# Kernel tuning notes

Measured on AMD Instinct MI355X. Metric: run time of the kernel, lower is better.

The kernel has to match this reference:

```python
import jax, jax.numpy as jnp
import numpy as np

N_USERS, N_ITEMS = 100000, 100000
N_NODES = N_USERS + N_ITEMS
N_EDGES = 4000000
USER_DIM, ITEM_DIM = 256, 128
COMMON, HIDDEN, OUT = 64, 64, 32


def setup_inputs() -> dict:
    key = jax.random.key(0)
    ks = jax.random.split(key, 12)
    inp = {
        "user_tensor": jax.random.normal(ks[0], (N_USERS, USER_DIM), jnp.float32),
        "item_tensor": jax.random.normal(ks[1], (N_ITEMS, ITEM_DIM), jnp.float32),
        "edge_index": jax.random.randint(ks[2], (2, N_EDGES), 0, N_NODES, jnp.int64),
        "edge_weight": jax.random.uniform(ks[3], (N_EDGES,), jnp.float32),
        # user_proj / item_proj (nn.Linear: y = x @ W + b)
        "Wu": jax.random.normal(ks[4], (USER_DIM, COMMON), jnp.float32) / np.sqrt(USER_DIM),
        "bu": jnp.zeros((COMMON,), jnp.float32),
        "Wi": jax.random.normal(ks[5], (ITEM_DIM, COMMON), jnp.float32) / np.sqrt(ITEM_DIM),
        "bi": jnp.zeros((COMMON,), jnp.float32),
        # GCNConv layers (linear without bias + separate bias)
        "W1": jax.random.normal(ks[6], (COMMON, HIDDEN), jnp.float32) / np.sqrt(COMMON),
        "b1": jnp.zeros((HIDDEN,), jnp.float32),
        "W2": jax.random.normal(ks[7], (HIDDEN, OUT), jnp.float32) / np.sqrt(HIDDEN),
        "b2": jnp.zeros((OUT,), jnp.float32),
    }
    return inp


def gcn_conv(x, W, b, src, dst, ew, num_nodes):
    """PyG GCNConv: add self-loops (weight 1), symmetric deg norm, transform, scatter-add."""
    x = x @ W  # transform first: [N, out]
    loop = jnp.arange(num_nodes, dtype=src.dtype)
    src2 = jnp.concatenate([src, loop])
    dst2 = jnp.concatenate([dst, loop])
    ew2 = jnp.concatenate([ew, jnp.ones((num_nodes,), x.dtype)])
    deg = jax.ops.segment_sum(ew2, dst2, num_segments=num_nodes)
    dinv = jnp.where(deg > 0, jax.lax.rsqrt(deg), 0.0)
    norm = dinv[src2] * ew2 * dinv[dst2]  # [E+N]
    msgs = x[src2] * norm[:, None]  # gather + scale: [E+N, out]
    return jax.ops.segment_sum(msgs, dst2, num_segments=num_nodes) + b


def reference(user_tensor, item_tensor, edge_index, edge_weight,
              Wu, bu, Wi, bi, W1, b1, W2, b2):
    user_emb = user_tensor @ Wu + bu
    item_emb = item_tensor @ Wi + bi
    x = jnp.concatenate([user_emb, item_emb], axis=0)  # [N_NODES, COMMON]
    src, dst = edge_index[0], edge_index[1]
    x = gcn_conv(x, W1, b1, src, dst, edge_weight, N_NODES)
    x = jax.nn.relu(x)
    x = gcn_conv(x, W2, b2, src, dst, edge_weight, N_NODES)
    return x
```

## Files before the change

kernel.cpp:

```cpp
#include <hip/hip_runtime.h>
#include <hip/hip_bf16.h>

#define N_USERS_C 100000
#define N_ITEMS_C 100000
#define N_NODES_C 200000
#define USER_DIM_C 256
#define ITEM_DIM_C 128
#define COMMON_C 64
#define HIDDEN_C 64
#define OUT_DIM_C 32

#define CB_BITS 8
#define CB_NODES 256
#define NCB ((N_NODES_C + CB_NODES - 1) / CB_NODES)
#define CB_CAP 5632
#define B_THREADS 256
#define B_UNROLL (CB_CAP / B_THREADS)

#define BIN_GRID 512
#define BIN_CHUNK_MAX 8192
#define MAX_EPT 8

typedef unsigned int uint32;
typedef __bf16 bf16x8 __attribute__((ext_vector_type(8)));
typedef float f32x4 __attribute__((ext_vector_type(4)));



__device__ __forceinline__ float bf2f(ushort u) { return __uint_as_float(((unsigned)u) << 16); }
__device__ __forceinline__ ushort f2bf(float f) {
    unsigned u = __float_as_uint(f);
    return (ushort)((u + 0x7FFFu + ((u >> 16) & 1u)) >> 16);
}
__device__ __forceinline__ void store4(float* p, float a, float b, float c, float d) {
    *(float4*)p = make_float4(a, b, c, d);
}
__device__ __forceinline__ void store4(ushort* p, float a, float b, float c, float d) {
    ushort4 u;
    u.x = f2bf(a); u.y = f2bf(b); u.z = f2bf(c); u.w = f2bf(d);
    *(ushort4*)p = u;
}

union ABFrag {
    uint4 q;
    ushort u[8];
    bf16x8 v;
};


__global__ __launch_bounds__(1024) void bin_kernel(const int* __restrict__ src,
                                                   const int* __restrict__ dst,
                                                   const float* __restrict__ ew,
                                                   int* __restrict__ bucket_cnt,
                                                   uint2* __restrict__ rec2, int E, int chunk) {
    __shared__ int hist[NCB];
    __shared__ int cur[NCB];
    for (int i = threadIdx.x; i < NCB; i += 1024) hist[i] = 0;
    __syncthreads();
    const int beg = blockIdx.x * chunk;
    const int end = min(E, beg + chunk);

    int dc[MAX_EPT];
#pragma unroll
    for (int s = 0; s < MAX_EPT / 4; ++s) {
        const int e0 = beg + (threadIdx.x << 2) + (s << 12);
        int4 d4 = make_int4(-1, -1, -1, -1);
        if (e0 + 3 < end) {
            d4 = *(const int4*)(dst + e0);
        } else if (e0 < end) {
            d4.x = dst[e0];
            if (e0 + 1 < end) d4.y = dst[e0 + 1];
            if (e0 + 2 < end) d4.z = dst[e0 + 2];
        }
        dc[s * 4 + 0] = d4.x; dc[s * 4 + 1] = d4.y;
        dc[s * 4 + 2] = d4.z; dc[s * 4 + 3] = d4.w;
        if (d4.x >= 0) atomicAdd(&hist[d4.x >> CB_BITS], 1);
        if (d4.y >= 0) atomicAdd(&hist[d4.y >> CB_BITS], 1);
        if (d4.z >= 0) atomicAdd(&hist[d4.z >> CB_BITS], 1);
        if (d4.w >= 0) atomicAdd(&hist[d4.w >> CB_BITS], 1);
    }
    __syncthreads();

    for (int i = threadIdx.x; i < NCB; i += 1024) {
        const int h = hist[i];
        cur[i] = h ? atomicAdd(&bucket_cnt[i], h) : 0;
    }
    __syncthreads();

#pragma unroll
    for (int s = 0; s < MAX_EPT / 4; ++s) {
        const int e0 = beg + (threadIdx.x << 2) + (s << 12);
        if (e0 >= end) continue;
        int4 s4;
        float4 w4;
        if (e0 + 3 < end) {
            s4 = *(const int4*)(src + e0);
            w4 = *(const float4*)(ew + e0);
        } else {
            s4 = make_int4(0, 0, 0, 0);
            w4 = make_float4(0, 0, 0, 0);
            s4.x = src[e0]; w4.x = ew[e0];
            if (e0 + 1 < end) { s4.y = src[e0 + 1]; w4.y = ew[e0 + 1]; }
            if (e0 + 2 < end) { s4.z = src[e0 + 2]; w4.z = ew[e0 + 2]; }
        }
        const int dv[4] = {dc[s * 4 + 0], dc[s * 4 + 1], dc[s * 4 + 2], dc[s * 4 + 3]};
        const int sv[4] = {s4.x, s4.y, s4.z, s4.w};
        const float wv[4] = {w4.x, w4.y, w4.z, w4.w};
#pragma unroll
        for (int k = 0; k < 4; ++k) {
            const int d = dv[k];
            if (d < 0) continue;
            uint32 q = (uint32)(wv[k] * 255.0f + 0.5f);
            if (q > 255u) q = 255u;
            const int b = d >> CB_BITS;
            const int slot = atomicAdd(&cur[b], 1);
            if (slot < CB_CAP)
                rec2[(size_t)b * CB_CAP + slot] =
                    make_uint2((((uint32)sv[k]) << 8) | q, (uint32)d);
        }
    }
}


__global__ __launch_bounds__(B_THREADS) void region_build_kernel(
        const uint2* __restrict__ rec2, const int* __restrict__ bucket_cnt,
        uint32* __restrict__ csr32, int* __restrict__ row_beg,
        int* __restrict__ row_cnt, float* __restrict__ dinv) {
    __shared__ int pk[CB_NODES];
    __shared__ int s[CB_NODES];
    __shared__ int cur[CB_NODES];
    const int cb = blockIdx.x;
    const int node0 = cb << CB_BITS;
    int total = bucket_cnt[cb];
    if (total > CB_CAP) total = CB_CAP;
    const uint2* r = rec2 + (size_t)cb * CB_CAP;

    pk[threadIdx.x] = 0;
    __syncthreads();

    uint2 rr[B_UNROLL];
#pragma unroll
    for (int u = 0; u < B_UNROLL; ++u) {
        const int j = threadIdx.x + u * B_THREADS;
        if (j < total) {
            rr[u] = r[j];
            atomicAdd(&pk[rr[u].y & (CB_NODES - 1)],
                      (int)((1u << 20) | (rr[u].x & 255u)));
        } else {
            rr[u] = make_uint2(0u, 0xFFFFFFFFu);
        }
    }
    __syncthreads();

    const int v = pk[threadIdx.x] >> 20;
    s[threadIdx.x] = v;
    __syncthreads();
#pragma unroll
    for (int off = 1; off < CB_NODES; off <<= 1) {
        const int t = (threadIdx.x >= off) ? s[threadIdx.x - off] : 0;
        __syncthreads();
        s[threadIdx.x] += t;
        __syncthreads();
    }
    {
        const int ex = s[threadIdx.x] - v;
        const int node = node0 + threadIdx.x;
        const int abs0 = cb * (2 * CB_CAP) + ex;
        if (node < N_NODES_C) {
            row_beg[node] = abs0;
            row_cnt[node] = v;
            dinv[node] = rsqrtf(1.0f + (float)(pk[threadIdx.x] & 0xFFFFF) * (1.0f / 255.0f));
        }
        cur[threadIdx.x] = abs0;
    }
    __syncthreads();

#pragma unroll
    for (int u = 0; u < B_UNROLL; ++u) {
        if (rr[u].y != 0xFFFFFFFFu) {
            const int slot = atomicAdd(&cur[rr[u].y & (CB_NODES - 1)], 1);
            csr32[slot] = rr[u].x;
        }
    }
}


__device__ __forceinline__ void wt_one(const float* W, ushort* WT, int K, int N, int i) {
    int k = i / N, n = i % N;
    WT[(size_t)n * K + k] = f2bf(W[i]);
}

__global__ void wt_prep_kernel(const float* __restrict__ Wu, const float* __restrict__ Wi,
                               const float* __restrict__ W1, const float* __restrict__ W2,
                               ushort* __restrict__ wtU, ushort* __restrict__ wtI,
                               ushort* __restrict__ wt1, ushort* __restrict__ wt2) {
    const int SU = USER_DIM_C * 64, SI = ITEM_DIM_C * 64, S1 = 64 * 64, S2 = 64 * 32;
    int i = blockIdx.x * blockDim.x + threadIdx.x;
    if (i < SU) { wt_one(Wu, wtU, USER_DIM_C, 64, i); return; }
    i -= SU;
    if (i < SI) { wt_one(Wi, wtI, ITEM_DIM_C, 64, i); return; }
    i -= SI;
    if (i < S1) { wt_one(W1, wt1, 64, 64, i); return; }
    i -= S1;
    if (i < S2) wt_one(W2, wt2, 64, 32, i);
}

template <int K, int NT, bool XF32, bool SCALE>
__global__ __launch_bounds__(256) void mfma_proj_kernel(const void* __restrict__ Xv,
                                                        const ushort* __restrict__ WT,
                                                        const float* __restrict__ bias,
                                                        const float* __restrict__ dinvp,
                                                        ushort* __restrict__ Y, int M) {
    const int lane = threadIdx.x & 63;
    const int wave = threadIdx.x >> 6;
    const int lr = lane & 15;
    const int quad = lane >> 4;
    const int m0 = blockIdx.x * 64 + wave * 16;
    const int N = NT * 16;

    f32x4 acc[NT];
#pragma unroll
    for (int nt = 0; nt < NT; ++nt) acc[nt] = (f32x4){0.0f, 0.0f, 0.0f, 0.0f};

    int arow = m0 + lr;
    if (arow >= M) arow = M - 1;
    const size_t abase = (size_t)arow * K;

    for (int kc = 0; kc < K; kc += 32) {
        const int k0 = kc + quad * 8;
        ABFrag a;
        if (XF32) {
            const float* Xf = (const float*)Xv;
            float4 x0 = *(const float4*)(Xf + abase + k0);
            float4 x1 = *(const float4*)(Xf + abase + k0 + 4);
            a.u[0] = f2bf(x0.x); a.u[1] = f2bf(x0.y); a.u[2] = f2bf(x0.z); a.u[3] = f2bf(x0.w);
            a.u[4] = f2bf(x1.x); a.u[5] = f2bf(x1.y); a.u[6] = f2bf(x1.z); a.u[7] = f2bf(x1.w);
        } else {
            const ushort* Xb = (const ushort*)Xv;
            a.q = *(const uint4*)(Xb + abase + k0);
        }
#pragma unroll
        for (int nt = 0; nt < NT; ++nt) {
            ABFrag bf;
            bf.q = *(const uint4*)(WT + (size_t)(nt * 16 + lr) * K + k0);
            acc[nt] = __builtin_amdgcn_mfma_f32_16x16x32_bf16(a.v, bf.v, acc[nt], 0, 0, 0);
        }
    }

#pragma unroll
    for (int r = 0; r < 4; ++r) {
        const int m = m0 + quad * 4 + r;
        if (m < M) {
            const float sc = SCALE ? dinvp[m] : 1.0f;
#pragma unroll
            for (int nt = 0; nt < NT; ++nt) {
                const int n = nt * 16 + lr;
                const float bc = bias ? bias[n] : 0.0f;
                Y[(size_t)m * N + n] = f2bf((acc[nt][r] + bc) * sc);
            }
        }
    }
}

template <int N, bool RELU, typename TY>
__global__ void gather_kernel(const int* __restrict__ row_beg, const int* __restrict__ row_cnt,
                              const uint32* __restrict__ csr, const ushort* __restrict__ y,
                              const float* __restrict__ dinv, const float* __restrict__ b,
                              TY* __restrict__ out) {
    constexpr int LPN = N / 4;
    const int node = blockIdx.x * (256 / LPN) + threadIdx.x / LPN;
    const int c0 = (threadIdx.x % LPN) * 4;

    const int beg = row_beg[node];
    const int end = beg + row_cnt[node];

    float a0[4] = {0, 0, 0, 0}, a1[4] = {0, 0, 0, 0}, a2[4] = {0, 0, 0, 0}, a3[4] = {0, 0, 0, 0};
    int j = beg;
    for (; j + 4 <= end; j += 4) {
        uint32 e0 = csr[j], e1 = csr[j + 1], e2 = csr[j + 2], e3 = csr[j + 3];
        int s0 = e0 >> 8, s1 = e1 >> 8, s2 = e2 >> 8, s3 = e3 >> 8;
        float c0v = (float)(e0 & 255u) * (1.0f / 255.0f);
        float c1v = (float)(e1 & 255u) * (1.0f / 255.0f);
        float c2v = (float)(e2 & 255u) * (1.0f / 255.0f);
        float c3v = (float)(e3 & 255u) * (1.0f / 255.0f);
        ushort4 u0 = *(const ushort4*)(y + (size_t)s0 * N + c0);
        ushort4 u1 = *(const ushort4*)(y + (size_t)s1 * N + c0);
        ushort4 u2 = *(const ushort4*)(y + (size_t)s2 * N + c0);
        ushort4 u3 = *(const ushort4*)(y + (size_t)s3 * N + c0);
        a0[0] += bf2f(u0.x) * c0v; a0[1] += bf2f(u0.y) * c0v;
        a0[2] += bf2f(u0.z) * c0v; a0[3] += bf2f(u0.w) * c0v;
        a1[0] += bf2f(u1.x) * c1v; a1[1] += bf2f(u1.y) * c1v;
        a1[2] += bf2f(u1.z) * c1v; a1[3] += bf2f(u1.w) * c1v;
        a2[0] += bf2f(u2.x) * c2v; a2[1] += bf2f(u2.y) * c2v;
        a2[2] += bf2f(u2.z) * c2v; a2[3] += bf2f(u2.w) * c2v;
        a3[0] += bf2f(u3.x) * c3v; a3[1] += bf2f(u3.y) * c3v;
        a3[2] += bf2f(u3.z) * c3v; a3[3] += bf2f(u3.w) * c3v;
    }
    for (; j < end; ++j) {
        uint32 e = csr[j];
        int s = e >> 8;
        float cv = (float)(e & 255u) * (1.0f / 255.0f);
        ushort4 u = *(const ushort4*)(y + (size_t)s * N + c0);
        a0[0] += bf2f(u.x) * cv; a0[1] += bf2f(u.y) * cv;
        a0[2] += bf2f(u.z) * cv; a0[3] += bf2f(u.w) * cv;
    }
    const float di = dinv[node];
    ushort4 us = *(const ushort4*)(y + (size_t)node * N + c0);
    float4 bc = *(const float4*)(b + c0);
    float r0 = (((a0[0] + a1[0]) + (a2[0] + a3[0])) + bf2f(us.x)) * di + bc.x;
    float r1 = (((a0[1] + a1[1]) + (a2[1] + a3[1])) + bf2f(us.y)) * di + bc.y;
    float r2 = (((a0[2] + a1[2]) + (a2[2] + a3[2])) + bf2f(us.z)) * di + bc.z;
    float r3 = (((a0[3] + a1[3]) + (a2[3] + a3[3])) + bf2f(us.w)) * di + bc.w;
    if (RELU) {
        r0 = fmaxf(r0, 0.0f); r1 = fmaxf(r1, 0.0f);
        r2 = fmaxf(r2, 0.0f); r3 = fmaxf(r3, 0.0f);
    }
    store4(&out[(size_t)node * N + c0], r0, r1, r2, r3);
}


extern "C" void kernel_launch(void* const* d_in, const int* in_sizes, int n_in,
                              void* d_out, int out_size, void* d_ws, size_t ws_size,
                              hipStream_t stream) {
    const float* user = (const float*)d_in[0];
    const float* item = (const float*)d_in[1];
    const int* ei = (const int*)d_in[2];
    const float* ew = (const float*)d_in[3];
    const float* Wu = (const float*)d_in[4];
    const float* bu = (const float*)d_in[5];
    const float* Wi = (const float*)d_in[6];
    const float* bi = (const float*)d_in[7];
    const float* W1 = (const float*)d_in[8];
    const float* b1 = (const float*)d_in[9];
    const float* W2 = (const float*)d_in[10];
    const float* b2 = (const float*)d_in[11];
    float* out = (float*)d_out;

    const int E = in_sizes[3];
    const int* src = ei;
    const int* dst = ei + E;
    const int NB = N_NODES_C;
    const int nblk = (E > BIN_GRID * BIN_CHUNK_MAX) ? ((E + BIN_CHUNK_MAX - 1) / BIN_CHUNK_MAX)
                                                    : BIN_GRID;
    const int chunk = (((E + nblk - 1) / nblk) + 3) & ~3;

    char* p = (char*)d_ws;
    uint2* rec2 = (uint2*)p;   p += (size_t)NCB * CB_CAP * 8;
    ushort* emb = (ushort*)p;  p += (size_t)NB * 64 * 2;
    ushort* y1 = (ushort*)p;   p += (size_t)NB * 64 * 2;
    ushort* h1 = (ushort*)p;   p += (size_t)NB * 64 * 2;
    ushort* y2 = (ushort*)p;   p += (size_t)NB * 32 * 2;
    int* bucket_cnt = (int*)p; p += (size_t)NCB * 4;
    int* row_beg = (int*)p;    p += (size_t)NB * 4;
    int* row_cnt = (int*)p;    p += (size_t)NB * 4;
    float* dinv = (float*)p;   p += (size_t)NB * 4;
    ushort* wtU = (ushort*)p;  p += (size_t)USER_DIM_C * 64 * 2;
    ushort* wtI = (ushort*)p;  p += (size_t)ITEM_DIM_C * 64 * 2;
    ushort* wt1 = (ushort*)p;  p += (size_t)64 * 64 * 2;
    ushort* wt2 = (ushort*)p;  p += (size_t)64 * 32 * 2;

    uint32* csr = (uint32*)rec2;

    hipMemsetAsync(bucket_cnt, 0, (size_t)NCB * 4, stream);
    bin_kernel<<<nblk, 1024, 0, stream>>>(src, dst, ew, bucket_cnt, rec2, E, chunk);
    region_build_kernel<<<NCB, B_THREADS, 0, stream>>>(rec2, bucket_cnt, csr, row_beg, row_cnt,
                                                       dinv);

    wt_prep_kernel<<<120, 256, 0, stream>>>(Wu, Wi, W1, W2, wtU, wtI, wt1, wt2);

    mfma_proj_kernel<USER_DIM_C, 4, true, false><<<(N_USERS_C + 63) / 64, 256, 0, stream>>>(
        user, wtU, bu, nullptr, emb, N_USERS_C);
    mfma_proj_kernel<ITEM_DIM_C, 4, true, false><<<(N_ITEMS_C + 63) / 64, 256, 0, stream>>>(
        item, wtI, bi, nullptr, emb + (size_t)N_USERS_C * 64, N_ITEMS_C);

    mfma_proj_kernel<64, 4, false, true><<<NB / 64, 256, 0, stream>>>(
        emb, wt1, (const float*)nullptr, dinv, y1, NB);
    gather_kernel<64, true><<<NB / 16, 256, 0, stream>>>(row_beg, row_cnt, csr, y1, dinv, b1, h1);

    mfma_proj_kernel<64, 2, false, true><<<NB / 64, 256, 0, stream>>>(
        h1, wt2, (const float*)nullptr, dinv, y2, NB);
    gather_kernel<32, false><<<NB / 32, 256, 0, stream>>>(row_beg, row_cnt, csr, y2, dinv, b2, out);
}
```

Baseline: 526.1 us.

## Fuse input projections with first GCN transform and fold weight prep into binning

Result: faster. 511.4 us (-2.8%).

```diff
diff --git a/kernel.cpp b/kernel.cpp
--- a/kernel.cpp
+++ b/kernel.cpp
@@ -21,6 +21,8 @@
 #define BIN_CHUNK_MAX 8192
 #define MAX_EPT 8
 
+#define UBLK 1563
+
 typedef unsigned int uint32;
 typedef __bf16 bf16x8 __attribute__((ext_vector_type(8)));
 typedef float f32x4 __attribute__((ext_vector_type(4)));
@@ -48,11 +50,31 @@
 };
 
 
-__global__ __launch_bounds__(1024) void bin_kernel(const int* __restrict__ src,
-                                                   const int* __restrict__ dst,
-                                                   const float* __restrict__ ew,
-                                                   int* __restrict__ bucket_cnt,
-                                                   uint2* __restrict__ rec2, int E, int chunk) {
+__device__ __forceinline__ void wt_one(const float* W, ushort* WT, int K, int N, int i) {
+    int k = i / N, n = i % N;
+    WT[(size_t)n * K + k] = f2bf(W[i]);
+}
+
+
+__global__ __launch_bounds__(1024) void bin_kernel(
+        const int* __restrict__ src, const int* __restrict__ dst,
+        const float* __restrict__ ew, int* __restrict__ bucket_cnt,
+        uint2* __restrict__ rec2, int E, int chunk,
+        const float* __restrict__ Wu, const float* __restrict__ Wi,
+        const float* __restrict__ W1, const float* __restrict__ W2,
+        ushort* __restrict__ wtU, ushort* __restrict__ wtI,
+        ushort* __restrict__ wt1, ushort* __restrict__ wt2) {
+    {
+        const int SU = USER_DIM_C * 64, SI = ITEM_DIM_C * 64, S1 = 64 * 64, S2 = 64 * 32;
+        int i = blockIdx.x * 1024 + threadIdx.x;
+        if (i < SU + SI + S1 + S2) {
+            if (i < SU) wt_one(Wu, wtU, USER_DIM_C, 64, i);
+            else if ((i -= SU) < SI) wt_one(Wi, wtI, ITEM_DIM_C, 64, i);
+            else if ((i -= SI) < S1) wt_one(W1, wt1, 64, 64, i);
+            else wt_one(W2, wt2, 64, 32, i - S1);
+        }
+    }
+
     __shared__ int hist[NCB];
     __shared__ int cur[NCB];
     for (int i = threadIdx.x; i < NCB; i += 1024) hist[i] = 0;
@@ -185,24 +207,92 @@
 }
 
 
-__device__ __forceinline__ void wt_one(const float* W, ushort* WT, int K, int N, int i) {
-    int k = i / N, n = i % N;
-    WT[(size_t)n * K + k] = f2bf(W[i]);
-}
-
-__global__ void wt_prep_kernel(const float* __restrict__ Wu, const float* __restrict__ Wi,
-                               const float* __restrict__ W1, const float* __restrict__ W2,
-                               ushort* __restrict__ wtU, ushort* __restrict__ wtI,
-                               ushort* __restrict__ wt1, ushort* __restrict__ wt2) {
-    const int SU = USER_DIM_C * 64, SI = ITEM_DIM_C * 64, S1 = 64 * 64, S2 = 64 * 32;
-    int i = blockIdx.x * blockDim.x + threadIdx.x;
-    if (i < SU) { wt_one(Wu, wtU, USER_DIM_C, 64, i); return; }
-    i -= SU;
-    if (i < SI) { wt_one(Wi, wtI, ITEM_DIM_C, 64, i); return; }
-    i -= SI;
-    if (i < S1) { wt_one(W1, wt1, 64, 64, i); return; }
-    i -= S1;
-    if (i < S2) wt_one(W2, wt2, 64, 32, i);
+__global__ __launch_bounds__(256) void fused_proj_kernel(
+        const float* __restrict__ user, const float* __restrict__ item,
+        const ushort* __restrict__ wtU, const ushort* __restrict__ wtI,
+        const ushort* __restrict__ wt1, const float* __restrict__ bu,
+        const float* __restrict__ bi, const float* __restrict__ dinv,
+        ushort* __restrict__ y1) {
+    __shared__ ushort elds[64][72];
+    const int lane = threadIdx.x & 63;
+    const int wave = threadIdx.x >> 6;
+    const int lr = lane & 15;
+    const int quad = lane >> 4;
+
+    const bool isUser = blockIdx.x < UBLK;
+    const int mb = isUser ? blockIdx.x : blockIdx.x - UBLK;
+    const int node0 = isUser ? 0 : N_USERS_C;
+    const float* X = isUser ? user : item;
+    const ushort* WT = isUser ? wtU : wtI;
+    const float* bias = isUser ? bu : bi;
+    const int K = isUser ? USER_DIM_C : ITEM_DIM_C;
+    const int M = N_USERS_C;
+
+    const int m0 = mb * 64 + wave * 16;
+
+    f32x4 acc[4];
+#pragma unroll
+    for (int nt = 0; nt < 4; ++nt) acc[nt] = (f32x4){0.0f, 0.0f, 0.0f, 0.0f};
+
+    int arow = m0 + lr;
+    if (arow >= M) arow = M - 1;
+    const float* Xr = X + (size_t)arow * K;
+
+    for (int kc = 0; kc < K; kc += 32) {
+        const int k0 = kc + quad * 8;
+        ABFrag a;
+        float4 x0 = *(const float4*)(Xr + k0);
+        float4 x1 = *(const float4*)(Xr + k0 + 4);
+        a.u[0] = f2bf(x0.x); a.u[1] = f2bf(x0.y); a.u[2] = f2bf(x0.z); a.u[3] = f2bf(x0.w);
+        a.u[4] = f2bf(x1.x); a.u[5] = f2bf(x1.y); a.u[6] = f2bf(x1.z); a.u[7] = f2bf(x1.w);
+#pragma unroll
+        for (int nt = 0; nt < 4; ++nt) {
+            ABFrag bf;
+            bf.q = *(const uint4*)(WT + (size_t)(nt * 16 + lr) * K + k0);
+            acc[nt] = __builtin_amdgcn_mfma_f32_16x16x32_bf16(a.v, bf.v, acc[nt], 0, 0, 0);
+        }
+    }
+
+#pragma unroll
+    for (int r = 0; r < 4; ++r) {
+        const int row_l = wave * 16 + quad * 4 + r;
+#pragma unroll
+        for (int nt = 0; nt < 4; ++nt) {
+            const int n = nt * 16 + lr;
+            elds[row_l][n] = f2bf(acc[nt][r] + bias[n]);
+        }
+    }
+    __syncthreads();
+
+    f32x4 acc2[4];
+#pragma unroll
+    for (int nt = 0; nt < 4; ++nt) acc2[nt] = (f32x4){0.0f, 0.0f, 0.0f, 0.0f};
+
+#pragma unroll
+    for (int kc = 0; kc < 64; kc += 32) {
+        const int k0 = kc + quad * 8;
+        ABFrag a;
+        a.q = *(const uint4*)(&elds[wave * 16 + lr][k0]);
+#pragma unroll
+        for (int nt = 0; nt < 4; ++nt) {
+            ABFrag bf;
+            bf.q = *(const uint4*)(wt1 + (size_t)(nt * 16 + lr) * 64 + k0);
+            acc2[nt] = __builtin_amdgcn_mfma_f32_16x16x32_bf16(a.v, bf.v, acc2[nt], 0, 0, 0);
+        }
+    }
+
+#pragma unroll
+    for (int r = 0; r < 4; ++r) {
+        const int m = m0 + quad * 4 + r;
+        if (m < M) {
+            const int node = node0 + m;
+            const float sc = dinv[node];
+#pragma unroll
+            for (int nt = 0; nt < 4; ++nt) {
+                y1[(size_t)node * 64 + nt * 16 + lr] = f2bf(acc2[nt][r] * sc);
+            }
+        }
+    }
 }
 
 template <int K, int NT, bool XF32, bool SCALE>
@@ -261,6 +351,7 @@
         }
     }
 }
+
 
 template <int N, bool RELU, typename TY>
 __global__ void gather_kernel(const int* __restrict__ row_beg, const int* __restrict__ row_cnt,
@@ -346,7 +437,6 @@
 
     char* p = (char*)d_ws;
     uint2* rec2 = (uint2*)p;   p += (size_t)NCB * CB_CAP * 8;
-    ushort* emb = (ushort*)p;  p += (size_t)NB * 64 * 2;
     ushort* y1 = (ushort*)p;   p += (size_t)NB * 64 * 2;
     ushort* h1 = (ushort*)p;   p += (size_t)NB * 64 * 2;
     ushort* y2 = (ushort*)p;   p += (size_t)NB * 32 * 2;
@@ -362,19 +452,13 @@
     uint32* csr = (uint32*)rec2;
 
     hipMemsetAsync(bucket_cnt, 0, (size_t)NCB * 4, stream);
-    bin_kernel<<<nblk, 1024, 0, stream>>>(src, dst, ew, bucket_cnt, rec2, E, chunk);
+    bin_kernel<<<nblk, 1024, 0, stream>>>(src, dst, ew, bucket_cnt, rec2, E, chunk,
+                                          Wu, Wi, W1, W2, wtU, wtI, wt1, wt2);
     region_build_kernel<<<NCB, B_THREADS, 0, stream>>>(rec2, bucket_cnt, csr, row_beg, row_cnt,
                                                        dinv);
 
-    wt_prep_kernel<<<120, 256, 0, stream>>>(Wu, Wi, W1, W2, wtU, wtI, wt1, wt2);
-
-    mfma_proj_kernel<USER_DIM_C, 4, true, false><<<(N_USERS_C + 63) / 64, 256, 0, stream>>>(
-        user, wtU, bu, nullptr, emb, N_USERS_C);
-    mfma_proj_kernel<ITEM_DIM_C, 4, true, false><<<(N_ITEMS_C + 63) / 64, 256, 0, stream>>>(
-        item, wtI, bi, nullptr, emb + (size_t)N_USERS_C * 64, N_ITEMS_C);
-
-    mfma_proj_kernel<64, 4, false, true><<<NB / 64, 256, 0, stream>>>(
-        emb, wt1, (const float*)nullptr, dinv, y1, NB);
+    fused_proj_kernel<<<2 * UBLK, 256, 0, stream>>>(user, item, wtU, wtI, wt1, bu, bi, dinv, y1);
+
     gather_kernel<64, true><<<NB / 16, 256, 0, stream>>>(row_beg, row_cnt, csr, y1, dinv, b1, h1);
 
     mfma_proj_kernel<64, 2, false, true><<<NB / 64, 256, 0, stream>>>(
```
